# Kernel tuning notes

Hardware: AMD Instinct MI355X
Metric: run time of the kernel (lower is better)

## Reference

```python
import jax, jax.numpy as jnp
import numpy as np

N, E, S = 50000, 800000, 3          # nodes, edges, message-passing steps
ND, ED, GD = 7, 4, 2                # raw node/edge/global feature dims
H, L = 64, 64                       # hidden and latent sizes


def _mlp3(x, W0, b0, W1, b1, W2, b2):
    # MLP([H, H, L]) with gelu between layers, none after last (dropout off).
    x = jax.nn.gelu(x @ W0 + b0)
    x = jax.nn.gelu(x @ W1 + b1)
    return x @ W2 + b2


def _ln(x, scale, bias, eps=1e-6):
    mu = jnp.mean(x, axis=-1, keepdims=True)
    xc = x - mu
    var = jnp.mean(xc * xc, axis=-1, keepdims=True)
    return xc * jax.lax.rsqrt(var + eps) * scale + bias


def setup_inputs() -> dict:
    key = jax.random.key(0)
    ks = iter(jax.random.split(key, 40))

    def W(i, o, stacked=False):
        shape = (S, i, o) if stacked else (i, o)
        return (jax.random.normal(next(ks), shape, jnp.float32) / np.sqrt(i)).astype(jnp.float32)

    inp = {
        "nodes": jax.random.normal(next(ks), (N, ND), jnp.float32),
        "edges": jax.random.normal(next(ks), (E, ED), jnp.float32),
        "glob": jax.random.normal(next(ks), (1, GD), jnp.float32),
        # node embedder MLP [H,H,L]
        "emb_n_W0": W(ND, H), "emb_n_b0": jnp.zeros((H,), jnp.float32),
        "emb_n_W1": W(H, H), "emb_n_b1": jnp.zeros((H,), jnp.float32),
        "emb_n_W2": W(H, L), "emb_n_b2": jnp.zeros((L,), jnp.float32),
        # edge embedder MLP
        "emb_e_W0": W(ED, H), "emb_e_b0": jnp.zeros((H,), jnp.float32),
        "emb_e_W1": W(H, H), "emb_e_b1": jnp.zeros((H,), jnp.float32),
        "emb_e_W2": W(H, L), "emb_e_b2": jnp.zeros((L,), jnp.float32),
        # per-step edge update MLP: in = edges(L)+senders(L)+receivers(L)+glob(GD)
        "edge_W0": W(3 * L + GD, H, True), "edge_b0": jnp.zeros((S, H), jnp.float32),
        "edge_W1": W(H, H, True), "edge_b1": jnp.zeros((S, H), jnp.float32),
        "edge_W2": W(H, L, True), "edge_b2": jnp.zeros((S, L), jnp.float32),
        # per-step node update MLP: in = nodes(L)+received(L)+glob(GD)
        "node_W0": W(2 * L + GD, H, True), "node_b0": jnp.zeros((S, H), jnp.float32),
        "node_W1": W(H, H, True), "node_b1": jnp.zeros((S, H), jnp.float32),
        "node_W2": W(H, L, True), "node_b2": jnp.zeros((S, L), jnp.float32),
        # per-step LayerNorms for nodes and edges
        "ln_n_scale": jnp.ones((S, L), jnp.float32), "ln_n_bias": jnp.zeros((S, L), jnp.float32),
        "ln_e_scale": jnp.ones((S, L), jnp.float32), "ln_e_bias": jnp.zeros((S, L), jnp.float32),
        # decoder MLP [H,H,3]
        "dec_W0": W(L, H), "dec_b0": jnp.zeros((H,), jnp.float32),
        "dec_W1": W(H, H), "dec_b1": jnp.zeros((H,), jnp.float32),
        "dec_W2": W(H, 3), "dec_b2": jnp.zeros((3,), jnp.float32),
        "senders": jax.random.randint(next(ks), (E,), 0, N),
        "receivers": jax.random.randint(next(ks), (E,), 0, N),
    }
    return inp


def reference(nodes, edges, glob,
              emb_n_W0, emb_n_b0, emb_n_W1, emb_n_b1, emb_n_W2, emb_n_b2,
              emb_e_W0, emb_e_b0, emb_e_W1, emb_e_b1, emb_e_W2, emb_e_b2,
              edge_W0, edge_b0, edge_W1, edge_b1, edge_W2, edge_b2,
              node_W0, node_b0, node_W1, node_b1, node_W2, node_b2,
              ln_n_scale, ln_n_bias, ln_e_scale, ln_e_bias,
              dec_W0, dec_b0, dec_W1, dec_b1, dec_W2, dec_b2,
              senders, receivers):
    # GraphMapFeatures embedder
    n = _mlp3(nodes, emb_n_W0, emb_n_b0, emb_n_W1, emb_n_b1, emb_n_W2, emb_n_b2)  # [N, L]
    e = _mlp3(edges, emb_e_W0, emb_e_b0, emb_e_W1, emb_e_b1, emb_e_W2, emb_e_b2)  # [E, L]
    n_nodes, n_edges = n.shape[0], e.shape[0]
    ge = jnp.broadcast_to(glob, (n_edges, glob.shape[1]))  # globals per edge (single graph)
    gn = jnp.broadcast_to(glob, (n_nodes, glob.shape[1]))  # globals per node
    steps = edge_W0.shape[0]
    for s in range(steps):
        # edge update: gather sender/receiver node feats, concat, MLP
        e_in = jnp.concatenate([e, n[senders], n[receivers], ge], axis=1)  # [E, 3L+GD]
        new_e = _mlp3(e_in, edge_W0[s], edge_b0[s], edge_W1[s], edge_b1[s], edge_W2[s], edge_b2[s])
        # scatter-aggregate to receivers (jraph default: segment_sum)
        recv = jax.ops.segment_sum(new_e, receivers, num_segments=n_nodes)  # [N, L]
        n_in = jnp.concatenate([n, recv, gn], axis=1)  # [N, 2L+GD]
        new_n = _mlp3(n_in, node_W0[s], node_b0[s], node_W1[s], node_b1[s], node_W2[s], node_b2[s])
        # residual skip connections then per-step LayerNorm
        n = _ln(n + new_n, ln_n_scale[s], ln_n_bias[s])
        e = _ln(e + new_e, ln_e_scale[s], ln_e_bias[s])
    # decoder on nodes -> [N, 3]
    return _mlp3(n, dec_W0, dec_b0, dec_W1, dec_b1, dec_W2, dec_b2)
```

## Files before the change

kernel.cpp:

```cpp
#include <hip/hip_runtime.h>

#define N_NODES 50000
#define N_EDGES 800000
#define NSTEPS 3
#define NBLK_SCAN 196

typedef __attribute__((ext_vector_type(8))) short bf16x8;
typedef __attribute__((ext_vector_type(4))) float f32x4;


__device__ __forceinline__ float ldf(const void* p, long i, int bf) {
    if (bf) {
        unsigned int u = ((const unsigned short*)p)[i];
        u <<= 16;
        return __uint_as_float(u);
    }
    return ((const float*)p)[i];
}

__device__ __forceinline__ unsigned short f2bf(float f) {
    unsigned int u = __float_as_uint(f);
    u = u + 0x7FFFu + ((u >> 16) & 1u);
    return (unsigned short)(u >> 16);
}

__device__ __forceinline__ float bf2f(unsigned short u) {
    return __uint_as_float(((unsigned int)u) << 16);
}

__device__ __forceinline__ float gelu_f(float x) {
    float x2 = x * x;
    float m = x * fmaf(-0.10294325f, x2, -2.30220847f);
    float e = __builtin_amdgcn_exp2f(m);
    return x * __builtin_amdgcn_rcpf(1.0f + e);
}

__device__ __forceinline__ void zero4(f32x4 a[4]) {
#pragma unroll
    for (int t = 0; t < 4; t++) a[t] = (f32x4){0.f, 0.f, 0.f, 0.f};
}

__device__ __forceinline__ void mfma_chunk(f32x4 acc[4], bf16x8 a, const unsigned short* bb) {
    acc[0] = __builtin_amdgcn_mfma_f32_16x16x32_bf16(a, *(const bf16x8*)(bb + 0), acc[0], 0, 0, 0);
    acc[1] = __builtin_amdgcn_mfma_f32_16x16x32_bf16(a, *(const bf16x8*)(bb + 512), acc[1], 0, 0, 0);
    acc[2] = __builtin_amdgcn_mfma_f32_16x16x32_bf16(a, *(const bf16x8*)(bb + 1024), acc[2], 0, 0, 0);
    acc[3] = __builtin_amdgcn_mfma_f32_16x16x32_bf16(a, *(const bf16x8*)(bb + 1536), acc[3], 0, 0, 0);
}

__global__ void detect_kernel(const void* probe, int* flag) {
    if (threadIdx.x == 0 && blockIdx.x == 0) {
        unsigned int w = *(const unsigned int*)probe;
        *flag = (w == 0x3F803F80u) ? 1 : 0;
    }
}

__global__ void hist_kernel(const int* __restrict__ receivers, int* __restrict__ counts) {
    int i = blockIdx.x * 256 + threadIdx.x;
    if (i < N_EDGES) atomicAdd(&counts[receivers[i]], 1);
}

__global__ void scan_partial(const int* __restrict__ counts, int* __restrict__ base,
                             int* __restrict__ blockSums) {
    __shared__ int sm[256];
    int b = blockIdx.x, t = threadIdx.x, i = b * 256 + t;
    int v = (i < N_NODES) ? counts[i] : 0;
    sm[t] = v;
    __syncthreads();
    for (int off = 1; off < 256; off <<= 1) {
        int x = (t >= off) ? sm[t - off] : 0;
        __syncthreads();
        sm[t] += x;
        __syncthreads();
    }
    if (i < N_NODES) base[i] = sm[t] - v;
    if (t == 255) blockSums[b] = sm[255];
}

__global__ void scan_tops(int* __restrict__ blockSums, int* __restrict__ tops) {
    __shared__ int sm[256];
    int t = threadIdx.x;
    int v = (t < NBLK_SCAN) ? blockSums[t] : 0;
    sm[t] = v;
    __syncthreads();
    for (int off = 1; off < 256; off <<= 1) {
        int x = (t >= off) ? sm[t - off] : 0;
        __syncthreads();
        sm[t] += x;
        __syncthreads();
    }
    if (t < NBLK_SCAN) tops[t] = sm[t] - v;
}

__global__ void scan_add(int* __restrict__ base, const int* __restrict__ tops,
                         int* __restrict__ cursor) {
    int b = blockIdx.x, i = b * 256 + threadIdx.x;
    if (i < N_NODES) {
        int v = base[i] + tops[b];
        base[i] = v;
        cursor[i] = v;
    }
}

__global__ void scatter_kernel(const int* __restrict__ senders,
                               const int* __restrict__ receivers, int* __restrict__ cursor,
                               int* __restrict__ ss, int* __restrict__ rsrt,
                               int* __restrict__ perm) {
    int i = blockIdx.x * 256 + threadIdx.x;
    if (i < N_EDGES) {
        int r = receivers[i];
        int pos = atomicAdd(&cursor[r], 1);
        ss[pos] = senders[i];
        rsrt[pos] = r;
        perm[pos] = i;
    }
}

struct PrepPtrs {
    const void* W[14];
    const void* eb0;
    const void* nb0;
    const void* glob;
};

#define PREP_WTOTAL 139264
__global__ void prep_all(PrepPtrs p, unsigned short* WbBase, float* b0eff_e, float* b0eff_n,
                         const int* __restrict__ flagp) {
    const int totals[14] = {36864, 12288, 12288, 24576, 12288, 12288, 2048,
                            4096,  4096,  2048,  4096,  4096,  4096,  4096};
    const int ksrc[14] = {192, 64, 64, 128, 64, 64, 7, 64, 64, 4, 64, 64, 64, 64};
    const int sstride[14] = {12416, 4096, 4096, 8320, 4096, 4096, 448,
                             4096,  4096, 256,  4096, 4096, 4096, 4096};
    const int nch[14] = {6, 2, 2, 4, 2, 2, 1, 2, 2, 1, 2, 2, 2, 2};

    const int bf = *flagp;
    int i = blockIdx.x * 256 + threadIdx.x;
    if (i < PREP_WTOTAL) {
        int e = 0, base = 0;
        while (i >= base + totals[e]) { base += totals[e]; e++; }
        int il = i - base;
        int j = il & 7, lane = (il >> 3) & 63, t = (il >> 9) & 3;
        int c = (il >> 11) % nch[e], s = il / (2048 * nch[e]);
        int k = c * 32 + (lane >> 4) * 8 + j;
        int col = t * 16 + (lane & 15);
        WbBase[i] = (k < ksrc[e]) ? f2bf(ldf(p.W[e], (long)s * sstride[e] + (long)k * 64 + col, bf))
                                  : (unsigned short)0;
    } else if (i < PREP_WTOTAL + 384) {
        int i2 = i - PREP_WTOTAL;
        float g0 = ldf(p.glob, 0, bf), g1 = ldf(p.glob, 1, bf);
        if (i2 < 192) {
            int s = i2 >> 6, col = i2 & 63;
            b0eff_e[i2] = ldf(p.eb0, i2, bf) + g0 * ldf(p.W[0], (long)s * 12416 + 192 * 64 + col, bf)
                                             + g1 * ldf(p.W[0], (long)s * 12416 + 193 * 64 + col, bf);
        } else {
            int il = i2 - 192;
            int s = il >> 6, col = il & 63;
            b0eff_n[il] = ldf(p.nb0, il, bf) + g0 * ldf(p.W[3], (long)s * 8320 + 128 * 64 + col, bf)
                                             + g1 * ldf(p.W[3], (long)s * 8320 + 129 * 64 + col, bf);
        }
    }
}

template <int DIN, int OUT_BF>
__global__ __launch_bounds__(256) void embed_mfma(
    const void* __restrict__ xin, const unsigned short* __restrict__ Wb0, const void* b0,
    const unsigned short* __restrict__ Wb1, const void* b1,
    const unsigned short* __restrict__ Wb2, const void* b2, void* __restrict__ outp,
    unsigned short* __restrict__ out_bf, const int* __restrict__ perm, int R,
    const int* __restrict__ flagp) {
    __shared__ __align__(16) unsigned short Xs[64 * 40];
    __shared__ __align__(16) unsigned short hbuf[64 * 72];
    const int bf = *flagp;
    const int tid = threadIdx.x;
    const long rb = (long)blockIdx.x * 64;
    {
        int r = tid >> 2, seg = tid & 3;
        long idx = rb + r;
        long src = (perm != nullptr && idx < R) ? (long)perm[idx] : idx;
        unsigned short u[8];
#pragma unroll
        for (int j = 0; j < 8; j++) {
            int col = seg * 8 + j;
            u[j] = (col < DIN && idx < R) ? f2bf(ldf(xin, src * DIN + col, bf)) : (unsigned short)0;
        }
        *(uint4*)&Xs[r * 40 + seg * 8] = *(uint4*)u;
    }
    __syncthreads();
    const int lane = tid & 63, w = tid >> 6, q = lane >> 4, l15 = lane & 15;
    const int arow = 16 * w + l15, aoff = q * 8;
    unsigned short* hw = hbuf + w * 16 * 72;

    f32x4 acc[4];
    zero4(acc);
    {
        bf16x8 a = *(const bf16x8*)&Xs[arow * 40 + aoff];
        mfma_chunk(acc, a, Wb0 + lane * 8);
#pragma unroll
        for (int t = 0; t < 4; t++) {
            int col = t * 16 + l15;
            float b = ldf(b0, col, bf);
#pragma unroll
            for (int reg = 0; reg < 4; reg++)
                hw[(q * 4 + reg) * 72 + col] = f2bf(gelu_f(acc[t][reg] + b));
        }
    }
    zero4(acc);
    {
#pragma unroll
        for (int c = 0; c < 2; c++) {
            bf16x8 a = *(const bf16x8*)&hw[l15 * 72 + c * 32 + aoff];
            mfma_chunk(acc, a, Wb1 + c * 2048 + lane * 8);
        }
#pragma unroll
        for (int t = 0; t < 4; t++) {
            int col = t * 16 + l15;
            float b = ldf(b1, col, bf);
#pragma unroll
            for (int reg = 0; reg < 4; reg++)
                hw[(q * 4 + reg) * 72 + col] = f2bf(gelu_f(acc[t][reg] + b));
        }
    }
    zero4(acc);
    {
#pragma unroll
        for (int c = 0; c < 2; c++) {
            bf16x8 a = *(const bf16x8*)&hw[l15 * 72 + c * 32 + aoff];
            mfma_chunk(acc, a, Wb2 + c * 2048 + lane * 8);
        }
    }
    if (OUT_BF) {
#pragma unroll
        for (int t = 0; t < 4; t++) {
            int col = t * 16 + l15;
            float b = ldf(b2, col, bf);
#pragma unroll
            for (int reg = 0; reg < 4; reg++)
                hw[(q * 4 + reg) * 72 + col] = f2bf(acc[t][reg] + b);
        }
        __syncthreads();
        for (int cc = tid; cc < 512; cc += 256) {
            int r = cc >> 3, seg = cc & 7;
            long idx = rb + r;
            if (idx < R)
                *(uint4*)&((unsigned short*)outp)[idx * 64 + seg * 8] =
                    *(const uint4*)&hbuf[r * 72 + seg * 8];
        }
    } else {
#pragma unroll
        for (int t = 0; t < 4; t++) {
            int col = t * 16 + l15;
            float b = ldf(b2, col, bf);
#pragma unroll
            for (int reg = 0; reg < 4; reg++) {
                long idx = rb + 16 * w + q * 4 + reg;
                if (idx < R) {
                    float v = acc[t][reg] + b;
                    ((float*)outp)[idx * 64 + col] = v;
                    out_bf[idx * 64 + col] = f2bf(v);
                }
            }
        }
    }
}

#define EST 72
__global__ __launch_bounds__(256) void edge_update_mfma(
    unsigned short* __restrict__ e_lat, const unsigned short* __restrict__ n_bf,
    const int* __restrict__ ss, const int* __restrict__ rsrt,
    const unsigned short* __restrict__ Wb0, const unsigned short* __restrict__ Wb1,
    const unsigned short* __restrict__ Wb2, const float* __restrict__ b0eff, const void* b1,
    const void* b2, const void* lnsc, const void* lnbi, float* __restrict__ recvbuf, int s,
    const int* __restrict__ flagp) {
    __shared__ __align__(16) unsigned short Ee[64 * EST];
    __shared__ __align__(16) unsigned short NsNr[128 * EST];
    __shared__ int rcvs[64];
    float* newe = (float*)NsNr;

    const int bf = *flagp;
    const int tid = threadIdx.x;
    const long rb = (long)blockIdx.x * 64;

    for (int c = tid; c < 512; c += 256) {
        int r = c >> 3, o = c & 7;
        *(uint4*)&Ee[r * EST + o * 8] = ((const uint4*)(e_lat + (rb + r) * 64))[o];
    }
    for (int c = tid; c < 1024; c += 256) {
        int part = c >> 9, r = (c >> 3) & 63, o = c & 7;
        long node = part ? rsrt[rb + r] : ss[rb + r];
        *(uint4*)&NsNr[(part * 64 + r) * EST + o * 8] = ((const uint4*)(n_bf + node * 64))[o];
    }
    if (tid < 64) rcvs[tid] = rsrt[rb + tid];
    __syncthreads();

    const int lane = tid & 63, w = tid >> 6, q = lane >> 4, l15 = lane & 15;
    const int arow = 16 * w + l15, aoff = q * 8;
    unsigned short* hw = Ee + w * 16 * EST;

    float ein[4][4];
#pragma unroll
    for (int reg = 0; reg < 4; reg++)
#pragma unroll
        for (int t = 0; t < 4; t++)
            ein[reg][t] = bf2f(Ee[(16 * w + q * 4 + reg) * EST + t * 16 + l15]);

    f32x4 acc[4];
    zero4(acc);
    {
        const unsigned short* B = Wb0 + (long)s * 6 * 2048 + lane * 8;
#pragma unroll
        for (int c = 0; c < 6; c++) {
            const unsigned short* src = (c < 2) ? Ee : (c < 4 ? NsNr : NsNr + 64 * EST);
            bf16x8 a = *(const bf16x8*)&src[arow * EST + (c & 1) * 32 + aoff];
            mfma_chunk(acc, a, B + c * 2048);
        }
#pragma unroll
        for (int t = 0; t < 4; t++) {
            const int col = t * 16 + l15;
            const float b = b0eff[s * 64 + col];
#pragma unroll
            for (int reg = 0; reg < 4; reg++)
                hw[(q * 4 + reg) * EST + col] = f2bf(gelu_f(acc[t][reg] + b));
        }
    }
    zero4(acc);
    {
        const unsigned short* B = Wb1 + (long)s * 2 * 2048 + lane * 8;
#pragma unroll
        for (int c = 0; c < 2; c++) {
            bf16x8 a = *(const bf16x8*)&hw[l15 * EST + c * 32 + aoff];
            mfma_chunk(acc, a, B + c * 2048);
        }
#pragma unroll
        for (int t = 0; t < 4; t++) {
            const int col = t * 16 + l15;
            const float b = ldf(b1, (long)s * 64 + col, bf);
#pragma unroll
            for (int reg = 0; reg < 4; reg++)
                hw[(q * 4 + reg) * EST + col] = f2bf(gelu_f(acc[t][reg] + b));
        }
    }
    zero4(acc);
    {
        const unsigned short* B = Wb2 + (long)s * 2 * 2048 + lane * 8;
#pragma unroll
        for (int c = 0; c < 2; c++) {
            bf16x8 a = *(const bf16x8*)&hw[l15 * EST + c * 32 + aoff];
            mfma_chunk(acc, a, B + c * 2048);
        }
    }
    __syncthreads();

    float fin[4][4];
#pragma unroll
    for (int t = 0; t < 4; t++) {
        const float b = ldf(b2, (long)s * 64 + t * 16 + l15, bf);
#pragma unroll
        for (int reg = 0; reg < 4; reg++) fin[reg][t] = acc[t][reg] + b;
    }
    float lsc[4], lbi[4];
#pragma unroll
    for (int t = 0; t < 4; t++) {
        lsc[t] = ldf(lnsc, (long)s * 64 + t * 16 + l15, bf);
        lbi[t] = ldf(lnbi, (long)s * 64 + t * 16 + l15, bf);
    }
#pragma unroll
    for (int reg = 0; reg < 4; reg++) {
        const int lr = q * 4 + reg;
        float u[4], ssum = 0.f;
#pragma unroll
        for (int t = 0; t < 4; t++) {
            newe[w * 1056 + lr * 66 + t * 16 + l15] = fin[reg][t];
            u[t] = ein[reg][t] + fin[reg][t];
            ssum += u[t];
        }
#pragma unroll
        for (int m = 1; m < 16; m <<= 1) ssum += __shfl_xor(ssum, m, 64);
        const float mu = ssum * (1.0f / 64.0f);
        float d[4], vv = 0.f;
#pragma unroll
        for (int t = 0; t < 4; t++) { d[t] = u[t] - mu; vv += d[t] * d[t]; }
#pragma unroll
        for (int m = 1; m < 16; m <<= 1) vv += __shfl_xor(vv, m, 64);
        const float rs = rsqrtf(vv * (1.0f / 64.0f) + 1e-6f);
#pragma unroll
        for (int t = 0; t < 4; t++)
            Ee[(16 * w + lr) * EST + t * 16 + l15] = f2bf(d[t] * rs * lsc[t] + lbi[t]);
    }
    __syncthreads();

    for (int cc = tid; cc < 512; cc += 256) {
        int r = cc >> 3, o = cc & 7;
        *(uint4*)&e_lat[(rb + r) * 64 + o * 8] = *(const uint4*)&Ee[r * EST + o * 8];
    }
    {
        const int col = tid & 63, g = tid >> 6;
        float a = 0.f;
#pragma unroll
        for (int rr = 0; rr < 16; rr++) {
            const int r = 16 * g + rr;
            a += newe[g * 1056 + rr * 66 + col];
            if (rr == 15 || rcvs[r + 1] != rcvs[r]) {
                atomicAdd(&recvbuf[(long)rcvs[r] * 64 + col], a);
                a = 0.f;
            }
        }
    }
}

#define NXS 136
__global__ __launch_bounds__(256) void node_update_mfma(
    float* __restrict__ n_lat, unsigned short* __restrict__ n_bf, float* __restrict__ recvbuf,
    const unsigned short* __restrict__ Wb0, const float* __restrict__ b0eff,
    const unsigned short* __restrict__ Wb1, const void* b1,
    const unsigned short* __restrict__ Wb2, const void* b2, const void* lnsc,
    const void* lnbi, int s, const int* __restrict__ flagp) {
    __shared__ __align__(16) unsigned short Xs[64 * NXS];
    __shared__ __align__(16) unsigned short hbuf[64 * 72];
    const int bf = *flagp;
    const int tid = threadIdx.x;
    const long rb = (long)blockIdx.x * 64;

    for (int cc = tid; cc < 512; cc += 256) {
        int r = cc >> 3, seg = cc & 7;
        long idx = rb + r;
        uint4 v = {0u, 0u, 0u, 0u};
        if (idx < N_NODES) v = ((const uint4*)(n_bf + idx * 64))[seg];
        *(uint4*)&Xs[r * NXS + seg * 8] = v;
    }
    for (int cc = tid; cc < 512; cc += 256) {
        int r = cc >> 3, seg = cc & 7;
        long idx = rb + r;
        unsigned short u[8] = {0, 0, 0, 0, 0, 0, 0, 0};
        if (idx < N_NODES) {
            const float* src = recvbuf + idx * 64 + seg * 8;
            float4 x0 = *(const float4*)src, x1 = *(const float4*)(src + 4);
            u[0] = f2bf(x0.x); u[1] = f2bf(x0.y); u[2] = f2bf(x0.z); u[3] = f2bf(x0.w);
            u[4] = f2bf(x1.x); u[5] = f2bf(x1.y); u[6] = f2bf(x1.z); u[7] = f2bf(x1.w);
        }
        *(uint4*)&Xs[r * NXS + 64 + seg * 8] = *(uint4*)u;
    }
    __syncthreads();

    const int lane = tid & 63, w = tid >> 6, q = lane >> 4, l15 = lane & 15;
    const int arow = 16 * w + l15, aoff = q * 8;
    unsigned short* hw = hbuf + w * 16 * 72;

    f32x4 acc[4];
    zero4(acc);
    {
        const unsigned short* B = Wb0 + (long)s * 4 * 2048 + lane * 8;
#pragma unroll
        for (int c = 0; c < 4; c++) {
            bf16x8 a = *(const bf16x8*)&Xs[arow * NXS + c * 32 + aoff];
            mfma_chunk(acc, a, B + c * 2048);
        }
#pragma unroll
        for (int t = 0; t < 4; t++) {
            const int col = t * 16 + l15;
            const float b = b0eff[s * 64 + col];
#pragma unroll
            for (int reg = 0; reg < 4; reg++)
                hw[(q * 4 + reg) * 72 + col] = f2bf(gelu_f(acc[t][reg] + b));
        }
    }
    zero4(acc);
    {
        const unsigned short* B = Wb1 + (long)s * 2 * 2048 + lane * 8;
#pragma unroll
        for (int c = 0; c < 2; c++) {
            bf16x8 a = *(const bf16x8*)&hw[l15 * 72 + c * 32 + aoff];
            mfma_chunk(acc, a, B + c * 2048);
        }
#pragma unroll
        for (int t = 0; t < 4; t++) {
            const int col = t * 16 + l15;
            const float b = ldf(b1, (long)s * 64 + col, bf);
#pragma unroll
            for (int reg = 0; reg < 4; reg++)
                hw[(q * 4 + reg) * 72 + col] = f2bf(gelu_f(acc[t][reg] + b));
        }
    }
    zero4(acc);
    {
        const unsigned short* B = Wb2 + (long)s * 2 * 2048 + lane * 8;
#pragma unroll
        for (int c = 0; c < 2; c++) {
            bf16x8 a = *(const bf16x8*)&hw[l15 * 72 + c * 32 + aoff];
            mfma_chunk(acc, a, B + c * 2048);
        }
    }
    float b2v[4], lsc[4], lbi[4];
#pragma unroll
    for (int t = 0; t < 4; t++) {
        b2v[t] = ldf(b2, (long)s * 64 + t * 16 + l15, bf);
        lsc[t] = ldf(lnsc, (long)s * 64 + t * 16 + l15, bf);
        lbi[t] = ldf(lnbi, (long)s * 64 + t * 16 + l15, bf);
    }
#pragma unroll
    for (int reg = 0; reg < 4; reg++) {
        const int rowl = 16 * w + q * 4 + reg;
        const long idx = rb + rowl;
        const bool valid = idx < N_NODES;
        float u[4], ssum = 0.f;
#pragma unroll
        for (int t = 0; t < 4; t++) {
            const int col = t * 16 + l15;
            float xn = valid ? n_lat[idx * 64 + col] : 0.f;
            u[t] = xn + acc[t][reg] + b2v[t];
            ssum += u[t];
        }
#pragma unroll
        for (int m = 1; m < 16; m <<= 1) ssum += __shfl_xor(ssum, m, 64);
        const float mu = ssum * (1.0f / 64.0f);
        float d[4], vv = 0.f;
#pragma unroll
        for (int t = 0; t < 4; t++) { d[t] = u[t] - mu; vv += d[t] * d[t]; }
#pragma unroll
        for (int m = 1; m < 16; m <<= 1) vv += __shfl_xor(vv, m, 64);
        const float rs = rsqrtf(vv * (1.0f / 64.0f) + 1e-6f);
        if (valid) {
#pragma unroll
            for (int t = 0; t < 4; t++) {
                const int col = t * 16 + l15;
                float v = d[t] * rs * lsc[t] + lbi[t];
                n_lat[idx * 64 + col] = v;
                n_bf[idx * 64 + col] = f2bf(v);
                recvbuf[idx * 64 + col] = 0.f;
            }
        }
    }
}

__global__ __launch_bounds__(256) void decoder_mfma(
    const unsigned short* __restrict__ n_bf, const unsigned short* __restrict__ Wb0,
    const void* b0, const unsigned short* __restrict__ Wb1, const void* b1, const void* W2,
    const void* b2, void* __restrict__ outp, const int* __restrict__ flagp) {
    __shared__ __align__(16) unsigned short Xs[64 * 72];
    __shared__ __align__(16) unsigned short hbuf[64 * 72];
    const int bf = *flagp;
    const int tid = threadIdx.x;
    const long rb = (long)blockIdx.x * 64;

    for (int cc = tid; cc < 512; cc += 256) {
        int r = cc >> 3, seg = cc & 7;
        long idx = rb + r;
        uint4 v = {0u, 0u, 0u, 0u};
        if (idx < N_NODES) v = ((const uint4*)(n_bf + idx * 64))[seg];
        *(uint4*)&Xs[r * 72 + seg * 8] = v;
    }
    __syncthreads();

    const int lane = tid & 63, w = tid >> 6, q = lane >> 4, l15 = lane & 15;
    const int arow = 16 * w + l15, aoff = q * 8;
    unsigned short* hw = hbuf + w * 16 * 72;

    f32x4 acc[4];
    zero4(acc);
    {
#pragma unroll
        for (int c = 0; c < 2; c++) {
            bf16x8 a = *(const bf16x8*)&Xs[arow * 72 + c * 32 + aoff];
            mfma_chunk(acc, a, Wb0 + c * 2048 + lane * 8);
        }
#pragma unroll
        for (int t = 0; t < 4; t++) {
            const int col = t * 16 + l15;
            const float b = ldf(b0, col, bf);
#pragma unroll
            for (int reg = 0; reg < 4; reg++)
                hw[(q * 4 + reg) * 72 + col] = f2bf(gelu_f(acc[t][reg] + b));
        }
    }
    zero4(acc);
    {
#pragma unroll
        for (int c = 0; c < 2; c++) {
            bf16x8 a = *(const bf16x8*)&hw[l15 * 72 + c * 32 + aoff];
            mfma_chunk(acc, a, Wb1 + c * 2048 + lane * 8);
        }
#pragma unroll
        for (int t = 0; t < 4; t++) {
            const int col = t * 16 + l15;
            const float b = ldf(b1, col, bf);
#pragma unroll
            for (int reg = 0; reg < 4; reg++)
                hw[(q * 4 + reg) * 72 + col] = f2bf(gelu_f(acc[t][reg] + b));
        }
    }
    const int col = tid & 63;
    const int r0 = (tid >> 6) * 16;
    if (col < 3) {
        float a[16];
        const float b = ldf(b2, col, bf);
#pragma unroll
        for (int i = 0; i < 16; i++) a[i] = b;
        for (int k = 0; k < 64; k++) {
            float wv = ldf(W2, (long)k * 3 + col, bf);
#pragma unroll
            for (int i = 0; i < 16; i++) a[i] = fmaf(bf2f(hbuf[(r0 + i) * 72 + k]), wv, a[i]);
        }
        for (int i = 0; i < 16; i++) {
            const long idx = rb + r0 + i;
            if (idx < N_NODES) {
                if (bf)
                    ((unsigned short*)outp)[idx * 3 + col] = f2bf(a[i]);
                else
                    ((float*)outp)[idx * 3 + col] = a[i];
            }
        }
    }
}

extern "C" void kernel_launch(void* const* d_in, const int* in_sizes, int n_in, void* d_out,
                              int out_size, void* d_ws, size_t ws_size, hipStream_t stream) {
    const void* nodes = d_in[0];
    const void* edges = d_in[1];
    const void* glob = d_in[2];
    const void *enW0 = d_in[3], *enb0 = d_in[4], *enW1 = d_in[5], *enb1 = d_in[6],
               *enW2 = d_in[7], *enb2 = d_in[8];
    const void *eeW0 = d_in[9], *eeb0 = d_in[10], *eeW1 = d_in[11], *eeb1 = d_in[12],
               *eeW2 = d_in[13], *eeb2 = d_in[14];
    const void *eW0 = d_in[15], *eb0 = d_in[16], *eW1 = d_in[17], *eb1 = d_in[18],
               *eW2 = d_in[19], *eb2 = d_in[20];
    const void *nW0 = d_in[21], *nb0 = d_in[22], *nW1 = d_in[23], *nb1 = d_in[24],
               *nW2 = d_in[25], *nb2 = d_in[26];
    const void *lnns = d_in[27], *lnnb = d_in[28], *lnes = d_in[29], *lneb = d_in[30];
    const void *dW0 = d_in[31], *db0 = d_in[32], *dW1 = d_in[33], *db1 = d_in[34],
               *dW2 = d_in[35], *db2 = d_in[36];
    const int* senders = (const int*)d_in[37];
    const int* receivers = (const int*)d_in[38];

    float* n_lat = (float*)d_ws;
    float* recvb = n_lat + 3200000;
    float* b0eff_e = recvb + 3200000;
    float* b0eff_n = b0eff_e + 192;
    int* flag = (int*)(b0eff_n + 192);
    unsigned short* e_lat = (unsigned short*)(b0eff_n + 256);
    unsigned short* n_bf = e_lat + 51200000;
    unsigned short* WbBase = n_bf + 3200000;
    unsigned short* WbE0 = WbBase;
    unsigned short* WbE1 = WbBase + 36864;
    unsigned short* WbE2 = WbBase + 49152;
    unsigned short* WbN0 = WbBase + 61440;
    unsigned short* WbN1 = WbBase + 86016;
    unsigned short* WbN2 = WbBase + 98304;
    unsigned short* WbNE0 = WbBase + 110592;
    unsigned short* WbNE1 = WbBase + 112640;
    unsigned short* WbNE2 = WbBase + 116736;
    unsigned short* WbEE0 = WbBase + 120832;
    unsigned short* WbEE1 = WbBase + 122880;
    unsigned short* WbEE2 = WbBase + 126976;
    unsigned short* WbD0 = WbBase + 131072;
    unsigned short* WbD1 = WbBase + 135168;
    int* counts = (int*)(WbBase + 139264 + 64);
    int* sbase = counts + N_NODES;
    int* cursor = sbase + N_NODES;
    int* blockSums = cursor + N_NODES;
    int* tops = blockSums + 256;
    int* ss = tops + 256;
    int* rsrt = ss + N_EDGES;
    int* perm = rsrt + N_EDGES;

    detect_kernel<<<1, 64, 0, stream>>>(lnns, flag);

    PrepPtrs pp;
    pp.W[0] = eW0;  pp.W[1] = eW1;  pp.W[2] = eW2;
    pp.W[3] = nW0;  pp.W[4] = nW1;  pp.W[5] = nW2;
    pp.W[6] = enW0; pp.W[7] = enW1; pp.W[8] = enW2;
    pp.W[9] = eeW0; pp.W[10] = eeW1; pp.W[11] = eeW2;
    pp.W[12] = dW0; pp.W[13] = dW1;
    pp.eb0 = eb0; pp.nb0 = nb0; pp.glob = glob;
    prep_all<<<(PREP_WTOTAL + 384 + 255) / 256, 256, 0, stream>>>(pp, WbBase, b0eff_e, b0eff_n,
                                                                  flag);
    hipMemsetAsync(recvb, 0, (size_t)N_NODES * 64 * sizeof(float), stream);
    hipMemsetAsync(counts, 0, (size_t)N_NODES * sizeof(int), stream);

    hist_kernel<<<(N_EDGES + 255) / 256, 256, 0, stream>>>(receivers, counts);
    scan_partial<<<NBLK_SCAN, 256, 0, stream>>>(counts, sbase, blockSums);
    scan_tops<<<1, 256, 0, stream>>>(blockSums, tops);
    scan_add<<<NBLK_SCAN, 256, 0, stream>>>(sbase, tops, cursor);
    scatter_kernel<<<(N_EDGES + 255) / 256, 256, 0, stream>>>(senders, receivers, cursor, ss,
                                                              rsrt, perm);

    embed_mfma<7, 0><<<(N_NODES + 63) / 64, 256, 0, stream>>>(
        nodes, WbNE0, enb0, WbNE1, enb1, WbNE2, enb2, n_lat, n_bf, (const int*)nullptr,
        N_NODES, flag);
    embed_mfma<4, 1><<<N_EDGES / 64, 256, 0, stream>>>(
        edges, WbEE0, eeb0, WbEE1, eeb1, WbEE2, eeb2, e_lat, (unsigned short*)nullptr, perm,
        N_EDGES, flag);
    for (int s = 0; s < NSTEPS; s++) {
        edge_update_mfma<<<N_EDGES / 64, 256, 0, stream>>>(
            e_lat, n_bf, ss, rsrt, WbE0, WbE1, WbE2, b0eff_e, eb1, eb2, lnes, lneb, recvb, s,
            flag);
        node_update_mfma<<<(N_NODES + 63) / 64, 256, 0, stream>>>(
            n_lat, n_bf, recvb, WbN0, b0eff_n, WbN1, nb1, WbN2, nb2, lnns, lnnb, s, flag);
    }
    decoder_mfma<<<(N_NODES + 63) / 64, 256, 0, stream>>>(n_bf, WbD0, db0, WbD1, db1, dW2,
                                                          db2, d_out, flag);
}
```

Measured before the change: 806.1 us.

## Fuse edge embedding MLP into first edge-update step kernel

The separate edge-embedding kernel, which wrote bf16 edge latents to global memory only to be reread by the first edge update, is removed. The embedding MLP now runs inside the step-0 edge update kernel, which reads raw edge features via the permutation and keeps the embedded latents in registers and shared memory. This saves a full write and read of the edge latent array and one launch, at the cost of a second kernel instantiation with more code. The shared-memory row stride is also reduced from 72 to 68.

```diff
diff --git a/kernel.cpp b/kernel.cpp
--- a/kernel.cpp
+++ b/kernel.cpp
@@ -160,13 +160,12 @@
     }
 }
 
-template <int DIN, int OUT_BF>
+template <int DIN>
 __global__ __launch_bounds__(256) void embed_mfma(
     const void* __restrict__ xin, const unsigned short* __restrict__ Wb0, const void* b0,
     const unsigned short* __restrict__ Wb1, const void* b1,
-    const unsigned short* __restrict__ Wb2, const void* b2, void* __restrict__ outp,
-    unsigned short* __restrict__ out_bf, const int* __restrict__ perm, int R,
-    const int* __restrict__ flagp) {
+    const unsigned short* __restrict__ Wb2, const void* b2, float* __restrict__ outp,
+    unsigned short* __restrict__ out_bf, int R, const int* __restrict__ flagp) {
     __shared__ __align__(16) unsigned short Xs[64 * 40];
     __shared__ __align__(16) unsigned short hbuf[64 * 72];
     const int bf = *flagp;
@@ -175,12 +174,11 @@
     {
         int r = tid >> 2, seg = tid & 3;
         long idx = rb + r;
-        long src = (perm != nullptr && idx < R) ? (long)perm[idx] : idx;
         unsigned short u[8];
 #pragma unroll
         for (int j = 0; j < 8; j++) {
             int col = seg * 8 + j;
-            u[j] = (col < DIN && idx < R) ? f2bf(ldf(xin, src * DIN + col, bf)) : (unsigned short)0;
+            u[j] = (col < DIN && idx < R) ? f2bf(ldf(xin, idx * DIN + col, bf)) : (unsigned short)0;
         }
         *(uint4*)&Xs[r * 40 + seg * 8] = *(uint4*)u;
     }
@@ -227,68 +225,62 @@
             mfma_chunk(acc, a, Wb2 + c * 2048 + lane * 8);
         }
     }
-    if (OUT_BF) {
-#pragma unroll
-        for (int t = 0; t < 4; t++) {
-            int col = t * 16 + l15;
-            float b = ldf(b2, col, bf);
-#pragma unroll
-            for (int reg = 0; reg < 4; reg++)
-                hw[(q * 4 + reg) * 72 + col] = f2bf(acc[t][reg] + b);
-        }
-        __syncthreads();
-        for (int cc = tid; cc < 512; cc += 256) {
-            int r = cc >> 3, seg = cc & 7;
-            long idx = rb + r;
-            if (idx < R)
-                *(uint4*)&((unsigned short*)outp)[idx * 64 + seg * 8] =
-                    *(const uint4*)&hbuf[r * 72 + seg * 8];
-        }
-    } else {
-#pragma unroll
-        for (int t = 0; t < 4; t++) {
-            int col = t * 16 + l15;
-            float b = ldf(b2, col, bf);
-#pragma unroll
-            for (int reg = 0; reg < 4; reg++) {
-                long idx = rb + 16 * w + q * 4 + reg;
-                if (idx < R) {
-                    float v = acc[t][reg] + b;
-                    ((float*)outp)[idx * 64 + col] = v;
-                    out_bf[idx * 64 + col] = f2bf(v);
-                }
-            }
-        }
-    }
-}
-
-#define EST 72
-__global__ __launch_bounds__(256) void edge_update_mfma(
-    unsigned short* __restrict__ e_lat, const unsigned short* __restrict__ n_bf,
-    const int* __restrict__ ss, const int* __restrict__ rsrt,
-    const unsigned short* __restrict__ Wb0, const unsigned short* __restrict__ Wb1,
-    const unsigned short* __restrict__ Wb2, const float* __restrict__ b0eff, const void* b1,
-    const void* b2, const void* lnsc, const void* lnbi, float* __restrict__ recvbuf, int s,
-    const int* __restrict__ flagp) {
+#pragma unroll
+    for (int t = 0; t < 4; t++) {
+        int col = t * 16 + l15;
+        float b = ldf(b2, col, bf);
+#pragma unroll
+        for (int reg = 0; reg < 4; reg++) {
+            long idx = rb + 16 * w + q * 4 + reg;
+            if (idx < R) {
+                float v = acc[t][reg] + b;
+                outp[idx * 64 + col] = v;
+                out_bf[idx * 64 + col] = f2bf(v);
+            }
+        }
+    }
+}
+
+#define EST 68
+struct EdgeP {
+    unsigned short* e_lat;
+    const unsigned short* n_bf;
+    const int* ss;
+    const int* rsrt;
+    const int* perm;
+    const void* xraw;
+    const unsigned short *Wb0, *Wb1, *Wb2;
+    const unsigned short *We0, *We1, *We2;
+    const void *eeb0, *eeb1, *eeb2;
+    const float* b0eff;
+    const void *b1, *b2, *lnsc, *lnbi;
+    float* recvbuf;
+    const int* flagp;
+};
+
+template <int EMBED>
+__global__ __launch_bounds__(256) void edge_update_mfma(EdgeP P, int s) {
     __shared__ __align__(16) unsigned short Ee[64 * EST];
     __shared__ __align__(16) unsigned short NsNr[128 * EST];
     __shared__ int rcvs[64];
     float* newe = (float*)NsNr;
 
-    const int bf = *flagp;
+    const int bf = *P.flagp;
     const int tid = threadIdx.x;
     const long rb = (long)blockIdx.x * 64;
 
-    for (int c = tid; c < 512; c += 256) {
-        int r = c >> 3, o = c & 7;
-        *(uint4*)&Ee[r * EST + o * 8] = ((const uint4*)(e_lat + (rb + r) * 64))[o];
+    if (!EMBED) {
+        for (int c = tid; c < 512; c += 256) {
+            int r = c >> 3, o = c & 7;
+            *(uint4*)&Ee[r * EST + o * 8] = ((const uint4*)(P.e_lat + (rb + r) * 64))[o];
+        }
     }
     for (int c = tid; c < 1024; c += 256) {
         int part = c >> 9, r = (c >> 3) & 63, o = c & 7;
-        long node = part ? rsrt[rb + r] : ss[rb + r];
-        *(uint4*)&NsNr[(part * 64 + r) * EST + o * 8] = ((const uint4*)(n_bf + node * 64))[o];
-    }
-    if (tid < 64) rcvs[tid] = rsrt[rb + tid];
+        long node = part ? P.rsrt[rb + r] : P.ss[rb + r];
+        *(uint4*)&NsNr[(part * 64 + r) * EST + o * 8] = ((const uint4*)(P.n_bf + node * 64))[o];
+    }
+    if (tid < 64) rcvs[tid] = P.rsrt[rb + tid];
     __syncthreads();
 
     const int lane = tid & 63, w = tid >> 6, q = lane >> 4, l15 = lane & 15;
@@ -296,16 +288,79 @@
     unsigned short* hw = Ee + w * 16 * EST;
 
     float ein[4][4];
-#pragma unroll
-    for (int reg = 0; reg < 4; reg++)
-#pragma unroll
-        for (int t = 0; t < 4; t++)
-            ein[reg][t] = bf2f(Ee[(16 * w + q * 4 + reg) * EST + t * 16 + l15]);
-
     f32x4 acc[4];
-    zero4(acc);
-    {
-        const unsigned short* B = Wb0 + (long)s * 6 * 2048 + lane * 8;
+
+    if (EMBED) {
+        unsigned short am[8] = {0, 0, 0, 0, 0, 0, 0, 0};
+        if (q == 0) {
+            long erow = P.perm[rb + 16 * w + l15];
+            if (bf) {
+                const unsigned short* xp = (const unsigned short*)P.xraw + erow * 4;
+                am[0] = xp[0]; am[1] = xp[1]; am[2] = xp[2]; am[3] = xp[3];
+            } else {
+                const float* xp = (const float*)P.xraw + erow * 4;
+                am[0] = f2bf(xp[0]); am[1] = f2bf(xp[1]);
+                am[2] = f2bf(xp[2]); am[3] = f2bf(xp[3]);
+            }
+        }
+        zero4(acc);
+        {
+            bf16x8 a0 = *(bf16x8*)am;
+            mfma_chunk(acc, a0, P.We0 + lane * 8);
+#pragma unroll
+            for (int t = 0; t < 4; t++) {
+                int col = t * 16 + l15;
+                float b = ldf(P.eeb0, col, bf);
+#pragma unroll
+                for (int reg = 0; reg < 4; reg++)
+                    hw[(q * 4 + reg) * EST + col] = f2bf(gelu_f(acc[t][reg] + b));
+            }
+        }
+        zero4(acc);
+        {
+#pragma unroll
+            for (int c = 0; c < 2; c++) {
+                bf16x8 a = *(const bf16x8*)&hw[l15 * EST + c * 32 + aoff];
+                mfma_chunk(acc, a, P.We1 + c * 2048 + lane * 8);
+            }
+#pragma unroll
+            for (int t = 0; t < 4; t++) {
+                int col = t * 16 + l15;
+                float b = ldf(P.eeb1, col, bf);
+#pragma unroll
+                for (int reg = 0; reg < 4; reg++)
+                    hw[(q * 4 + reg) * EST + col] = f2bf(gelu_f(acc[t][reg] + b));
+            }
+        }
+        zero4(acc);
+        {
+#pragma unroll
+            for (int c = 0; c < 2; c++) {
+                bf16x8 a = *(const bf16x8*)&hw[l15 * EST + c * 32 + aoff];
+                mfma_chunk(acc, a, P.We2 + c * 2048 + lane * 8);
+            }
+        }
+#pragma unroll
+        for (int t = 0; t < 4; t++) {
+            int col = t * 16 + l15;
+            float b = ldf(P.eeb2, col, bf);
+#pragma unroll
+            for (int reg = 0; reg < 4; reg++) {
+                ein[reg][t] = acc[t][reg] + b;
+                Ee[(16 * w + q * 4 + reg) * EST + col] = f2bf(ein[reg][t]);
+            }
+        }
+    } else {
+#pragma unroll
+        for (int reg = 0; reg < 4; reg++)
+#pragma unroll
+            for (int t = 0; t < 4; t++)
+                ein[reg][t] = bf2f(Ee[(16 * w + q * 4 + reg) * EST + t * 16 + l15]);
+    }
+
+    zero4(acc);
+    {
+        const unsigned short* B = P.Wb0 + (long)s * 6 * 2048 + lane * 8;
 #pragma unroll
         for (int c = 0; c < 6; c++) {
             const unsigned short* src = (c < 2) ? Ee : (c < 4 ? NsNr : NsNr + 64 * EST);
@@ -315,7 +370,7 @@
 #pragma unroll
         for (int t = 0; t < 4; t++) {
             const int col = t * 16 + l15;
-            const float b = b0eff[s * 64 + col];
+            const float b = P.b0eff[s * 64 + col];
 #pragma unroll
             for (int reg = 0; reg < 4; reg++)
                 hw[(q * 4 + reg) * EST + col] = f2bf(gelu_f(acc[t][reg] + b));
@@ -323,7 +378,7 @@
     }
     zero4(acc);
     {
-        const unsigned short* B = Wb1 + (long)s * 2 * 2048 + lane * 8;
+        const unsigned short* B = P.Wb1 + (long)s * 2 * 2048 + lane * 8;
 #pragma unroll
         for (int c = 0; c < 2; c++) {
             bf16x8 a = *(const bf16x8*)&hw[l15 * EST + c * 32 + aoff];
@@ -332,7 +387,7 @@
 #pragma unroll
         for (int t = 0; t < 4; t++) {
             const int col = t * 16 + l15;
-            const float b = ldf(b1, (long)s * 64 + col, bf);
+            const float b = ldf(P.b1, (long)s * 64 + col, bf);
 #pragma unroll
             for (int reg = 0; reg < 4; reg++)
                 hw[(q * 4 + reg) * EST + col] = f2bf(gelu_f(acc[t][reg] + b));
@@ -340,7 +395,7 @@
     }
     zero4(acc);
     {
-        const unsigned short* B = Wb2 + (long)s * 2 * 2048 + lane * 8;
+        const unsigned short* B = P.Wb2 + (long)s * 2 * 2048 + lane * 8;
 #pragma unroll
         for (int c = 0; c < 2; c++) {
             bf16x8 a = *(const bf16x8*)&hw[l15 * EST + c * 32 + aoff];
@@ -352,15 +407,15 @@
     float fin[4][4];
 #pragma unroll
     for (int t = 0; t < 4; t++) {
-        const float b = ldf(b2, (long)s * 64 + t * 16 + l15, bf);
+        const float b = ldf(P.b2, (long)s * 64 + t * 16 + l15, bf);
 #pragma unroll
         for (int reg = 0; reg < 4; reg++) fin[reg][t] = acc[t][reg] + b;
     }
     float lsc[4], lbi[4];
 #pragma unroll
     for (int t = 0; t < 4; t++) {
-        lsc[t] = ldf(lnsc, (long)s * 64 + t * 16 + l15, bf);
-        lbi[t] = ldf(lnbi, (long)s * 64 + t * 16 + l15, bf);
+        lsc[t] = ldf(P.lnsc, (long)s * 64 + t * 16 + l15, bf);
+        lbi[t] = ldf(P.lnbi, (long)s * 64 + t * 16 + l15, bf);
     }
 #pragma unroll
     for (int reg = 0; reg < 4; reg++) {
@@ -389,7 +444,7 @@
 
     for (int cc = tid; cc < 512; cc += 256) {
         int r = cc >> 3, o = cc & 7;
-        *(uint4*)&e_lat[(rb + r) * 64 + o * 8] = *(const uint4*)&Ee[r * EST + o * 8];
+        *(uint4*)&P.e_lat[(rb + r) * 64 + o * 8] = *(const uint4*)&Ee[r * EST + o * 8];
     }
     {
         const int col = tid & 63, g = tid >> 6;
@@ -399,7 +454,7 @@
             const int r = 16 * g + rr;
             a += newe[g * 1056 + rr * 66 + col];
             if (rr == 15 || rcvs[r + 1] != rcvs[r]) {
-                atomicAdd(&recvbuf[(long)rcvs[r] * 64 + col], a);
+                atomicAdd(&P.recvbuf[(long)rcvs[r] * 64 + col], a);
                 a = 0.f;
             }
         }
@@ -681,16 +736,23 @@
     scatter_kernel<<<(N_EDGES + 255) / 256, 256, 0, stream>>>(senders, receivers, cursor, ss,
                                                               rsrt, perm);
 
-    embed_mfma<7, 0><<<(N_NODES + 63) / 64, 256, 0, stream>>>(
-        nodes, WbNE0, enb0, WbNE1, enb1, WbNE2, enb2, n_lat, n_bf, (const int*)nullptr,
-        N_NODES, flag);
-    embed_mfma<4, 1><<<N_EDGES / 64, 256, 0, stream>>>(
-        edges, WbEE0, eeb0, WbEE1, eeb1, WbEE2, eeb2, e_lat, (unsigned short*)nullptr, perm,
-        N_EDGES, flag);
+    embed_mfma<7><<<(N_NODES + 63) / 64, 256, 0, stream>>>(
+        nodes, WbNE0, enb0, WbNE1, enb1, WbNE2, enb2, n_lat, n_bf, N_NODES, flag);
+
+    EdgeP ep;
+    ep.e_lat = e_lat; ep.n_bf = n_bf; ep.ss = ss; ep.rsrt = rsrt; ep.perm = perm;
+    ep.xraw = edges;
+    ep.Wb0 = WbE0; ep.Wb1 = WbE1; ep.Wb2 = WbE2;
+    ep.We0 = WbEE0; ep.We1 = WbEE1; ep.We2 = WbEE2;
+    ep.eeb0 = eeb0; ep.eeb1 = eeb1; ep.eeb2 = eeb2;
+    ep.b0eff = b0eff_e; ep.b1 = eb1; ep.b2 = eb2; ep.lnsc = lnes; ep.lnbi = lneb;
+    ep.recvbuf = recvb; ep.flagp = flag;
+
     for (int s = 0; s < NSTEPS; s++) {
-        edge_update_mfma<<<N_EDGES / 64, 256, 0, stream>>>(
-            e_lat, n_bf, ss, rsrt, WbE0, WbE1, WbE2, b0eff_e, eb1, eb2, lnes, lneb, recvb, s,
-            flag);
+        if (s == 0)
+            edge_update_mfma<1><<<N_EDGES / 64, 256, 0, stream>>>(ep, s);
+        else
+            edge_update_mfma<0><<<N_EDGES / 64, 256, 0, stream>>>(ep, s);
         node_update_mfma<<<(N_NODES + 63) / 64, 256, 0, stream>>>(
             n_lat, n_bf, recvb, WbN0, b0eff_n, WbN1, nb1, WbN2, nb2, lnns, lnnb, s, flag);
     }
```

Measured after the change: 860.7 us. +6.8%, slower.
